# Kernel tuning notes

Measured on AMD Instinct MI355X. Metric: run time of the kernel, lower is better.

## Reference

```python
import jax, jax.numpy as jnp
import numpy as np
from jax import lax

CORR = 16  # corr_size in the original module


def _adaptive_pool16(x):
    # exact adaptive avg pool when H, W divisible by 16 (torch-equivalent)
    B, C, H, W = x.shape
    return x.reshape(B, C, CORR, H // CORR, CORR, W // CORR).mean(axis=(3, 5))


def _l2_normalize(x, eps=1e-12):
    # torch F.normalize default: L2 over dim=1, norm clamped to eps
    n = jnp.sqrt(jnp.sum(x * x, axis=1, keepdims=True))
    return x / jnp.maximum(n, eps)


def _instance_norm(x, eps=1e-5):
    # InstanceNorm2d, affine=False, biased variance over H,W per (b,c)
    mu = x.mean(axis=(2, 3), keepdims=True)
    var = jnp.mean((x - mu) ** 2, axis=(2, 3), keepdims=True)
    return (x - mu) * lax.rsqrt(var + eps)


def _corr_reduce(x, W1, b1, W2, b2):
    # 1x1 conv (256 -> fc) + bias
    y = jnp.einsum('bchw,oc->bohw', x, W1[:, :, 0, 0]) + b1[None, :, None, None]
    y = jax.nn.relu(_instance_norm(y))
    # 3x3 conv, padding=1, stride=1
    y = lax.conv_general_dilated(y, W2, (1, 1), 'SAME',
                                 dimension_numbers=('NCHW', 'OIHW', 'NCHW'))
    return y + b2[None, :, None, None]


def _corr(feat):
    # pooled [B,C,16,16] used as per-sample bank of 256 1x1 conv kernels
    pooled = _adaptive_pool16(feat)                      # [B,C,16,16]
    norm = _l2_normalize(feat)                           # [B,C,H,W]
    B, C = pooled.shape[:2]
    ker = pooled.reshape(B, C, CORR * CORR)              # [B,C,256]
    # corr[b,p,h,w] = sum_c ker[b,c,p] * norm[b,c,h,w]
    return jnp.einsum('bcp,bchw->bphw', ker, norm)


def setup_inputs() -> dict:
    key = jax.random.key(0)
    ks = jax.random.split(key, 6)
    B, C, H, W = 16, 256, 96, 96
    fc = 256
    return {
        'F_infrared': jax.random.normal(ks[0], (B, C, H, W), jnp.float32),
        'F_visible': jax.random.normal(ks[1], (B, C, H, W), jnp.float32),
        'W1': jax.random.normal(ks[2], (fc, CORR * CORR, 1, 1), jnp.float32) * 0.05,
        'b1': jax.random.normal(ks[3], (fc,), jnp.float32) * 0.05,
        'W2': jax.random.normal(ks[4], (fc, fc, 3, 3), jnp.float32) * 0.05,
        'b2': jax.random.normal(ks[5], (fc,), jnp.float32) * 0.05,
    }


def reference(F_infrared, F_visible, W1, b1, W2, b2):
    VIS_corr = _corr_reduce(_corr(F_visible), W1, b1, W2, b2)
    IR_corr = _corr_reduce(_corr(F_infrared), W1, b1, W2, b2)
    return (IR_corr, VIS_corr)
```

## Files before the change

kernel.cpp:

```cpp
#include <hip/hip_runtime.h>
#include <hip/hip_bf16.h>

#define BATCH 16
#define CH    256
#define HH    96
#define WW    96
#define HWSZ  9216
#define FCH   256
#define PP    256

typedef float f32x4 __attribute__((ext_vector_type(4)));
typedef short bf16x8 __attribute__((ext_vector_type(8)));
typedef unsigned short ushortT;

#define APAD_ELEMS 2458624
#define APAD_CHUNKS 307328

__device__ __forceinline__ void gload16(const void* g, void* l) {
    __builtin_amdgcn_global_load_lds((const __attribute__((address_space(1))) void*)g,
                                     (__attribute__((address_space(3))) void*)l, 16, 0, 0);
}
__device__ __forceinline__ float bfu2f(ushortT u) {
    return __uint_as_float(((unsigned)u) << 16);
}
__device__ __forceinline__ ushortT f2bfu(float f) {
    __hip_bfloat16 hb = __float2bfloat16(f);
    return *reinterpret_cast<ushortT*>(&hb);
}

__global__ void fpack_k(const float* __restrict__ feat, ushortT* __restrict__ fpack,
                        float* __restrict__ rnorm)
{
    int b = blockIdx.y;
    int hw = blockIdx.x * 256 + threadIdx.x;
    const float* src = feat + (size_t)b * CH * HWSZ + hw;
    uint4* dst = (uint4*)fpack + (size_t)b * 32 * HWSZ + hw;
    float ss = 0.f;
    for (int cb = 0; cb < 32; ++cb) {
        union { ushortT u[8]; uint4 v; } pk;
#pragma unroll
        for (int i = 0; i < 8; ++i) {
            float v = src[(size_t)(cb * 8 + i) * HWSZ];
            ss += v * v;
            pk.u[i] = f2bfu(v);
        }
        dst[(size_t)cb * HWSZ] = pk.v;
    }
    rnorm[b * HWSZ + hw] = 1.0f / fmaxf(sqrtf(ss), 1e-12f);
}

__global__ void pool16b_k(const ushortT* __restrict__ fpack, float* __restrict__ pooled)
{
    int cb = blockIdx.x, b = blockIdx.y;
    const uint4* fp = (const uint4*)fpack + ((size_t)b * 32 + cb) * HWSZ;
    int t = threadIdx.x;
    int pr = t >> 4, pc = t & 15;
    float s[8] = {};
#pragma unroll
    for (int i = 0; i < 6; ++i) {
#pragma unroll
        for (int j = 0; j < 6; ++j) {
            uint4 v = fp[(pr * 6 + i) * WW + pc * 6 + j];
            const ushortT* u = (const ushortT*)&v;
#pragma unroll
            for (int k = 0; k < 8; ++k) s[k] += bfu2f(u[k]);
        }
    }
#pragma unroll
    for (int k = 0; k < 8; ++k)
        pooled[((size_t)b * CH + cb * 8 + k) * PP + t] = s[k] * (1.0f / 36.0f);
}

__global__ void gemmM_k(const float* __restrict__ W1, const float* __restrict__ pooled,
                        ushortT* __restrict__ Mb16)
{
    int b = blockIdx.z;
    int o0 = blockIdx.y * 16, c0 = blockIdx.x * 16;
    int ty = threadIdx.y, tx = threadIdx.x;
    __shared__ float Ws[16][17], Ps[16][17];
    float acc = 0.f;
    for (int p0 = 0; p0 < PP; p0 += 16) {
        Ws[ty][tx] = W1[(o0 + ty) * PP + p0 + tx];
        Ps[ty][tx] = pooled[((size_t)b * CH + (c0 + ty)) * PP + p0 + tx];
        __syncthreads();
#pragma unroll
        for (int p = 0; p < 16; ++p) acc += Ws[ty][p] * Ps[tx][p];
        __syncthreads();
    }
    int c = c0 + tx, o = o0 + ty;
    Mb16[(((size_t)b * 32 + (c >> 3)) * 256 + o) * 8 + (c & 7)] = f2bfu(acc);
}

__global__ void repack_w2_k(const float* __restrict__ W2, ushortT* __restrict__ W2r2)
{
    int e = blockIdx.x * 256 + threadIdx.x;
    int ci = e & 7, o = (e >> 3) & 255, cb = (e >> 11) & 31, s = e >> 16;
    int c = cb * 8 + ci;
    W2r2[e] = f2bfu(W2[((size_t)o * 256 + c) * 9 + s]);
}

__global__ void zborder_k(uint4* __restrict__ apad)
{
    int bl = blockIdx.x;
    uint4* apC = apad + (size_t)bl * APAD_CHUNKS;
    uint4 z; z.x = 0; z.y = 0; z.z = 0; z.w = 0;
    for (int e = threadIdx.x; e < 3136; e += 256) {
        apC[e] = z;
        apC[(size_t)97 * 32 * 98 + e] = z;
    }
    for (int e = threadIdx.x; e < 3072; e += 256) {
        int row = 1 + (e >> 5), cb = e & 31;
        size_t base = (size_t)(row * 32 + cb) * 98;
        apC[base] = z;
        apC[base + 97] = z;
    }
}

__global__ __launch_bounds__(256, 4) void gemmYm_k(const ushortT* __restrict__ Mb16,
                                                   const ushortT* __restrict__ fpack,
                                                   const float* __restrict__ rnorm,
                                                   ushortT* __restrict__ apad, int b0)
{
    int bl = blockIdx.z, bg = b0 + bl;
    int hw0 = blockIdx.x * 128;
    int o0 = blockIdx.y * 128;
    int tid = threadIdx.x, wave = tid >> 6, lane = tid & 63;
    int wm = wave >> 1, wn = wave & 1;
    int lr = lane & 15, kb = lane >> 4;

    __shared__ __align__(16) char smem[33280];

    const uint4* MbC = (const uint4*)Mb16 + (size_t)bg * 32 * 256;
    const uint4* fpC = (const uint4*)fpack + (size_t)bg * 32 * HWSZ;

    f32x4 acc[4][4] = {};

    auto STAGE = [&](int buf, int s) {
        int cb0 = s * 4;
        uint4* A = (uint4*)smem + (size_t)buf * 1024;
        uint4* B = A + 512;
#pragma unroll
        for (int i = 0; i < 2; ++i) {
            int e = tid + i * 256;
            int kk = e >> 7, j = e & 127;
            gload16(MbC + (size_t)(cb0 + kk) * 256 + o0 + j, A + e);
            gload16(fpC + (size_t)(cb0 + kk) * HWSZ + hw0 + j, B + e);
        }
    };

    STAGE(0, 0);
    for (int s = 0; s < 8; ++s) {
        int buf = s & 1;
        __syncthreads();
        if (s < 7) STAGE(buf ^ 1, s + 1);
        const bf16x8* AsV = (const bf16x8*)(smem + (size_t)buf * 16384);
        const bf16x8* BsV = AsV + 512;
        bf16x8 af[4], bfv[4];
#pragma unroll
        for (int mf = 0; mf < 4; ++mf) af[mf] = AsV[kb * 128 + wm * 64 + mf * 16 + lr];
#pragma unroll
        for (int nf = 0; nf < 4; ++nf) bfv[nf] = BsV[kb * 128 + wn * 64 + nf * 16 + lr];
#pragma unroll
        for (int mf = 0; mf < 4; ++mf)
#pragma unroll
            for (int nf = 0; nf < 4; ++nf)
                acc[mf][nf] = __builtin_amdgcn_mfma_f32_16x16x32_bf16(af[mf], bfv[nf], acc[mf][nf], 0, 0, 0);
    }
    __syncthreads();

    float rn[4];
#pragma unroll
    for (int nf = 0; nf < 4; ++nf)
        rn[nf] = rnorm[(size_t)bg * HWSZ + hw0 + wn * 64 + nf * 16 + lr];

    ushortT* T = (ushortT*)smem;
#pragma unroll
    for (int mf = 0; mf < 4; ++mf)
#pragma unroll
        for (int nf = 0; nf < 4; ++nf)
#pragma unroll
            for (int r = 0; r < 4; ++r)
                T[(wn * 64 + nf * 16 + lr) * 130 + wm * 64 + mf * 16 + kb * 4 + r] =
                    f2bfu(acc[mf][nf][r] * rn[nf]);
    __syncthreads();

    uint4* apC = (uint4*)apad + (size_t)bl * APAD_CHUNKS;
    int ob0 = blockIdx.y * 16;
#pragma unroll
    for (int i = 0; i < 8; ++i) {
        int e = tid + i * 256;
        int hw_l = e >> 4, ob = e & 15;
        uint4 v = *(uint4*)&T[hw_l * 130 + ob * 8];
        int hw = hw0 + hw_l;
        int h = hw / 96, w = hw - h * 96;
        apC[(size_t)((h + 1) * 32 + ob0 + ob) * 98 + (w + 1)] = v;
    }
}

__global__ void instats2_k(const ushortT* __restrict__ apad, float* __restrict__ mu,
                           float* __restrict__ istd)
{
    int ob = blockIdx.x, bl = blockIdx.y;
    const uint4* apC = (const uint4*)apad + (size_t)bl * APAD_CHUNKS;
    float s[8] = {}, s2[8] = {};
    for (int e = threadIdx.x; e < HWSZ; e += 256) {
        int row = e / 96;
        int w = e - row * 96;
        uint4 v = apC[(size_t)((row + 1) * 32 + ob) * 98 + w + 1];
        const ushortT* u = (const ushortT*)&v;
#pragma unroll
        for (int k = 0; k < 8; ++k) {
            float f = bfu2f(u[k]);
            s[k] += f; s2[k] += f * f;
        }
    }
#pragma unroll
    for (int off = 32; off > 0; off >>= 1) {
#pragma unroll
        for (int k = 0; k < 8; ++k) {
            s[k]  += __shfl_down(s[k],  off, 64);
            s2[k] += __shfl_down(s2[k], off, 64);
        }
    }
    __shared__ float sh[4][16];
    int wid = threadIdx.x >> 6;
    if ((threadIdx.x & 63) == 0) {
#pragma unroll
        for (int k = 0; k < 8; ++k) { sh[wid][k] = s[k]; sh[wid][8 + k] = s2[k]; }
    }
    __syncthreads();
    if (threadIdx.x < 8) {
        int k = threadIdx.x;
        float S  = sh[0][k] + sh[1][k] + sh[2][k] + sh[3][k];
        float S2 = sh[0][8 + k] + sh[1][8 + k] + sh[2][8 + k] + sh[3][8 + k];
        float m   = S * (1.0f / HWSZ);
        float var = S2 * (1.0f / HWSZ) - m * m;
        if (var < 0.f) var = 0.f;
        mu[bl * 256 + ob * 8 + k]   = m;
        istd[bl * 256 + ob * 8 + k] = rsqrtf(var + 1e-5f);
    }
}

__global__ void nr_k(ushortT* __restrict__ apad, const float* __restrict__ mu,
                     const float* __restrict__ istd)
{
    int row = blockIdx.x + 1, bl = blockIdx.y;
    __shared__ float smu[256], sis[256];
    smu[threadIdx.x] = mu[bl * 256 + threadIdx.x];
    sis[threadIdx.x] = istd[bl * 256 + threadIdx.x];
    __syncthreads();
    uint4* apC = (uint4*)apad + (size_t)bl * APAD_CHUNKS + (size_t)row * 32 * 98;
    for (int e = threadIdx.x; e < 3072; e += 256) {
        int ob = e / 96;
        int w = e - ob * 96 + 1;
        uint4 v = apC[(size_t)ob * 98 + w];
        ushortT* u = (ushortT*)&v;
#pragma unroll
        for (int k = 0; k < 8; ++k) {
            float f = (bfu2f(u[k]) - smu[ob * 8 + k]) * sis[ob * 8 + k];
            u[k] = f2bfu(f > 0.f ? f : 0.f);
        }
        apC[(size_t)ob * 98 + w] = v;
    }
}

__global__ __launch_bounds__(256, 2) void conv3m4_k(const ushortT* __restrict__ apad,
                                                    const ushortT* __restrict__ W2r2,
                                                    const float* __restrict__ b2,
                                                    float* __restrict__ out)
{
    int h0 = blockIdx.x * 4;
    int o0 = blockIdx.y * 64;
    int bl = blockIdx.z;
    int tid = threadIdx.x;
    int wave = tid >> 6, lane = tid & 63;
    int lr = lane & 15, kb = lane >> 4;

    __shared__ __align__(16) uint4 AsC[2304];
    __shared__ __align__(16) uint4 BsC[2560];

    const uint4* apadC = (const uint4*)apad + (size_t)bl * APAD_CHUNKS;
    const uint4* w2C   = (const uint4*)W2r2;
    const bf16x8* AsV = (const bf16x8*)AsC;
    const bf16x8* BsV = (const bf16x8*)BsC;

    f32x4 acc[4][6] = {};

    for (int ci = 0; ci < 8; ++ci) {
        int cb0 = ci * 4;
        __syncthreads();
#pragma unroll
        for (int i = 0; i < 9; ++i) {
            int e = tid + i * 256;
            int o = e & 63, kk = (e >> 6) & 3, s = e >> 8;
            gload16(w2C + (size_t)(s * 32 + cb0 + kk) * 256 + o0 + o, &AsC[e]);
        }
#pragma unroll
        for (int i = 0; i < 10; ++i) {
            int e = tid + i * 256;
            int se = e < 2352 ? e : e - 256;
            int w = se % 98, r = se / 98;
            int kk = r & 3, row = r >> 2;
            gload16(apadC + (size_t)((h0 + row) * 32 + cb0 + kk) * 98 + w, &BsC[e]);
        }
        __syncthreads();
#pragma unroll
        for (int kh = 0; kh < 3; ++kh) {
#pragma unroll
            for (int kw = 0; kw < 3; ++kw) {
                int s = kh * 3 + kw;
                bf16x8 af[4];
#pragma unroll
                for (int mf = 0; mf < 4; ++mf)
                    af[mf] = AsV[(s * 4 + kb) * 64 + mf * 16 + lr];
#pragma unroll
                for (int nf = 0; nf < 6; ++nf) {
                    bf16x8 bfr = BsV[((wave + kh) * 4 + kb) * 98 + nf * 16 + lr + kw];
#pragma unroll
                    for (int mf = 0; mf < 4; ++mf)
                        acc[mf][nf] = __builtin_amdgcn_mfma_f32_16x16x32_bf16(af[mf], bfr, acc[mf][nf], 0, 0, 0);
                }
            }
        }
    }

    int h = h0 + wave;
    float* obase = out + (size_t)bl * FCH * HWSZ + (size_t)h * WW;
#pragma unroll
    for (int mf = 0; mf < 4; ++mf) {
#pragma unroll
        for (int r = 0; r < 4; ++r) {
            int o = o0 + mf * 16 + kb * 4 + r;
            float bias = b2[o];
            float* orow = obase + (size_t)o * HWSZ;
#pragma unroll
            for (int nf = 0; nf < 6; ++nf)
                orow[nf * 16 + lr] = acc[mf][nf][r] + bias;
        }
    }
}

extern "C" void kernel_launch(void* const* d_in, const int* in_sizes, int n_in,
                              void* d_out, int out_size, void* d_ws, size_t ws_size,
                              hipStream_t stream)
{
    const float* Fir  = (const float*)d_in[0];
    const float* Fvis = (const float*)d_in[1];
    const float* W1   = (const float*)d_in[2];
    const float* W2   = (const float*)d_in[4];
    const float* b2   = (const float*)d_in[5];
    float* out = (float*)d_out;

    char* w = (char*)d_ws;
    const size_t poolB = (size_t)BATCH * CH * PP * 4;
    const size_t MbB   = (size_t)BATCH * 32 * 256 * 8 * 2;
    const size_t rnB   = (size_t)BATCH * HWSZ * 4;
    const size_t stB   = (size_t)BATCH * FCH * 4;
    const size_t w2rB  = (size_t)9 * 32 * 256 * 8 * 2;
    const size_t fpB   = (size_t)BATCH * 32 * HWSZ * 8 * 2;

    size_t off = 0;
    float*   pooled = (float*)(w + off);   off += poolB;
    ushortT* Mb16   = (ushortT*)(w + off); off += MbB;
    float*   rnorm  = (float*)(w + off);   off += rnB;
    float*   mu     = (float*)(w + off);   off += stB;
    float*   istd   = (float*)(w + off);   off += stB;
    ushortT* W2r2   = (ushortT*)(w + off); off += w2rB;
    ushortT* fpack  = (ushortT*)(w + off); off += fpB;
    const size_t fixed = off;

    const size_t apadB = (size_t)APAD_ELEMS * 2;
    size_t avail = ws_size > fixed ? ws_size - fixed : 0;
    int NB = (int)(avail / apadB);
    if (NB > BATCH) NB = BATCH;
    if (NB < 1) NB = 1;
    ushortT* apad = (ushortT*)(w + fixed);

    repack_w2_k<<<2304, 256, 0, stream>>>(W2, W2r2);
    zborder_k<<<NB, 256, 0, stream>>>((uint4*)apad);

    for (int f = 0; f < 2; ++f) {
        const float* feat = (f == 0) ? Fir : Fvis;
        float* o_ = out + (size_t)f * BATCH * FCH * HWSZ;

        fpack_k<<<dim3(36, BATCH), 256, 0, stream>>>(feat, fpack, rnorm);
        pool16b_k<<<dim3(32, BATCH), 256, 0, stream>>>(fpack, pooled);
        gemmM_k<<<dim3(16, 16, BATCH), dim3(16, 16), 0, stream>>>(W1, pooled, Mb16);

        for (int b0 = 0; b0 < BATCH; b0 += NB) {
            int nb = BATCH - b0 < NB ? BATCH - b0 : NB;
            gemmYm_k<<<dim3(72, 2, nb), 256, 0, stream>>>(Mb16, fpack, rnorm, apad, b0);
            instats2_k<<<dim3(32, nb), 256, 0, stream>>>(apad, mu, istd);
            nr_k<<<dim3(96, nb), 256, 0, stream>>>(apad, mu, istd);
            conv3m4_k<<<dim3(24, 4, nb), 256, 0, stream>>>(apad, W2r2, b2,
                                                           o_ + (size_t)b0 * FCH * HWSZ);
        }
    }
}
```

Before: 637.4 us.

## Fuse instance-norm stats into GEMM epilogue, load conv weights to registers, swizzle blocks

The GEMM epilogue now writes per-tile partial sums and sums of squares, which a small finalize kernel reduces. This replaces the separate stats kernel that re-read the whole padded activation buffer. The 3x3 conv kernel stops staging weights in LDS and loads them straight from global memory into registers per kh, which reduces LDS use but adds global loads inside the inner loop. It also remaps block indices so each XCD works on two batches, for L2 locality. Stats are now computed from fp32 values before bf16 rounding, which changes numerics slightly.

```diff
diff --git a/kernel.cpp b/kernel.cpp
--- a/kernel.cpp
+++ b/kernel.cpp
@@ -119,7 +119,9 @@
 __global__ __launch_bounds__(256, 4) void gemmYm_k(const ushortT* __restrict__ Mb16,
                                                    const ushortT* __restrict__ fpack,
                                                    const float* __restrict__ rnorm,
-                                                   ushortT* __restrict__ apad, int b0)
+                                                   ushortT* __restrict__ apad,
+                                                   float* __restrict__ ps,
+                                                   float* __restrict__ ps2, int b0)
 {
     int bl = blockIdx.z, bg = b0 + bl;
     int hw0 = blockIdx.x * 128;
@@ -173,6 +175,39 @@
     for (int nf = 0; nf < 4; ++nf)
         rn[nf] = rnorm[(size_t)bg * HWSZ + hw0 + wn * 64 + nf * 16 + lr];
 
+    {
+        float sA[4][4], sB[4][4];
+#pragma unroll
+        for (int mf = 0; mf < 4; ++mf)
+#pragma unroll
+            for (int r = 0; r < 4; ++r) {
+                float s1 = 0.f, s2 = 0.f;
+#pragma unroll
+                for (int nf = 0; nf < 4; ++nf) {
+                    float v = acc[mf][nf][r] * rn[nf];
+                    s1 += v; s2 += v * v;
+                }
+#pragma unroll
+                for (int off = 8; off > 0; off >>= 1) {
+                    s1 += __shfl_down(s1, off, 16);
+                    s2 += __shfl_down(s2, off, 16);
+                }
+                sA[mf][r] = s1; sB[mf][r] = s2;
+            }
+        if (lr == 0) {
+            int col = blockIdx.x * 2 + wn;
+#pragma unroll
+            for (int mf = 0; mf < 4; ++mf)
+#pragma unroll
+                for (int r = 0; r < 4; ++r) {
+                    int og = o0 + wm * 64 + mf * 16 + kb * 4 + r;
+                    size_t idx = ((size_t)bl * 256 + og) * 144 + col;
+                    ps[idx]  = sA[mf][r];
+                    ps2[idx] = sB[mf][r];
+                }
+        }
+    }
+
     ushortT* T = (ushortT*)smem;
 #pragma unroll
     for (int mf = 0; mf < 4; ++mf)
@@ -197,48 +232,19 @@
     }
 }
 
-__global__ void instats2_k(const ushortT* __restrict__ apad, float* __restrict__ mu,
-                           float* __restrict__ istd)
-{
-    int ob = blockIdx.x, bl = blockIdx.y;
-    const uint4* apC = (const uint4*)apad + (size_t)bl * APAD_CHUNKS;
-    float s[8] = {}, s2[8] = {};
-    for (int e = threadIdx.x; e < HWSZ; e += 256) {
-        int row = e / 96;
-        int w = e - row * 96;
-        uint4 v = apC[(size_t)((row + 1) * 32 + ob) * 98 + w + 1];
-        const ushortT* u = (const ushortT*)&v;
-#pragma unroll
-        for (int k = 0; k < 8; ++k) {
-            float f = bfu2f(u[k]);
-            s[k] += f; s2[k] += f * f;
-        }
-    }
-#pragma unroll
-    for (int off = 32; off > 0; off >>= 1) {
-#pragma unroll
-        for (int k = 0; k < 8; ++k) {
-            s[k]  += __shfl_down(s[k],  off, 64);
-            s2[k] += __shfl_down(s2[k], off, 64);
-        }
-    }
-    __shared__ float sh[4][16];
-    int wid = threadIdx.x >> 6;
-    if ((threadIdx.x & 63) == 0) {
-#pragma unroll
-        for (int k = 0; k < 8; ++k) { sh[wid][k] = s[k]; sh[wid][8 + k] = s2[k]; }
-    }
-    __syncthreads();
-    if (threadIdx.x < 8) {
-        int k = threadIdx.x;
-        float S  = sh[0][k] + sh[1][k] + sh[2][k] + sh[3][k];
-        float S2 = sh[0][8 + k] + sh[1][8 + k] + sh[2][8 + k] + sh[3][8 + k];
-        float m   = S * (1.0f / HWSZ);
-        float var = S2 * (1.0f / HWSZ) - m * m;
-        if (var < 0.f) var = 0.f;
-        mu[bl * 256 + ob * 8 + k]   = m;
-        istd[bl * 256 + ob * 8 + k] = rsqrtf(var + 1e-5f);
-    }
+__global__ void finstats_k(const float* __restrict__ ps, const float* __restrict__ ps2,
+                           float* __restrict__ mu, float* __restrict__ istd)
+{
+    int bl = blockIdx.x, o = threadIdx.x;
+    const float* p1 = ps  + ((size_t)bl * 256 + o) * 144;
+    const float* p2 = ps2 + ((size_t)bl * 256 + o) * 144;
+    float S = 0.f, S2 = 0.f;
+    for (int i = 0; i < 144; ++i) { S += p1[i]; S2 += p2[i]; }
+    float m   = S * (1.0f / HWSZ);
+    float var = S2 * (1.0f / HWSZ) - m * m;
+    if (var < 0.f) var = 0.f;
+    mu[bl * 256 + o]   = m;
+    istd[bl * 256 + o] = rsqrtf(var + 1e-5f);
 }
 
 __global__ void nr_k(ushortT* __restrict__ apad, const float* __restrict__ mu,
@@ -264,61 +270,66 @@
     }
 }
 
-__global__ __launch_bounds__(256, 2) void conv3m4_k(const ushortT* __restrict__ apad,
+__global__ __launch_bounds__(256, 2) void conv3m7_k(const ushortT* __restrict__ apad,
                                                     const ushortT* __restrict__ W2r2,
                                                     const float* __restrict__ b2,
-                                                    float* __restrict__ out)
-{
-    int h0 = blockIdx.x * 4;
-    int o0 = blockIdx.y * 64;
-    int bl = blockIdx.z;
+                                                    float* __restrict__ out, int swz)
+{
+    int ht, ot, bl;
+    if (swz) {
+        int lin = blockIdx.x + 24 * (blockIdx.y + 4 * blockIdx.z);
+        int xcd = lin & 7, i = lin >> 3;
+        int second = (i >= 96) ? 1 : 0;
+        bl = 2 * xcd + second;
+        int w = i - second * 96;
+        ot = w / 24; ht = w - ot * 24;
+    } else {
+        ht = blockIdx.x; ot = blockIdx.y; bl = blockIdx.z;
+    }
+    int h0 = ht * 4;
+    int o0 = ot * 64;
     int tid = threadIdx.x;
     int wave = tid >> 6, lane = tid & 63;
     int lr = lane & 15, kb = lane >> 4;
 
-    __shared__ __align__(16) uint4 AsC[2304];
     __shared__ __align__(16) uint4 BsC[2560];
 
     const uint4* apadC = (const uint4*)apad + (size_t)bl * APAD_CHUNKS;
-    const uint4* w2C   = (const uint4*)W2r2;
-    const bf16x8* AsV = (const bf16x8*)AsC;
-    const bf16x8* BsV = (const bf16x8*)BsC;
+    const bf16x8* w2V  = (const bf16x8*)W2r2;
+    const bf16x8* BsV  = (const bf16x8*)BsC;
 
     f32x4 acc[4][6] = {};
 
     for (int ci = 0; ci < 8; ++ci) {
         int cb0 = ci * 4;
         __syncthreads();
-#pragma unroll
-        for (int i = 0; i < 9; ++i) {
-            int e = tid + i * 256;
-            int o = e & 63, kk = (e >> 6) & 3, s = e >> 8;
-            gload16(w2C + (size_t)(s * 32 + cb0 + kk) * 256 + o0 + o, &AsC[e]);
-        }
 #pragma unroll
         for (int i = 0; i < 10; ++i) {
             int e = tid + i * 256;
             int se = e < 2352 ? e : e - 256;
             int w = se % 98, r = se / 98;
             int kk = r & 3, row = r >> 2;
-            gload16(apadC + (size_t)((h0 + row) * 32 + cb0 + kk) * 98 + w, &BsC[e]);
+            gload16(apadC + (size_t)((h0 + row) * 32 + cb0 + kk) * 98 + w,
+                    &BsC[e]);
         }
         __syncthreads();
-#pragma unroll
+#pragma unroll 1
         for (int kh = 0; kh < 3; ++kh) {
+            bf16x8 aR[3][4];
+#pragma unroll
+            for (int kw = 0; kw < 3; ++kw)
+#pragma unroll
+                for (int mf = 0; mf < 4; ++mf)
+                    aR[kw][mf] = w2V[(size_t)((kh * 3 + kw) * 32 + cb0 + kb) * 256
+                                     + o0 + mf * 16 + lr];
 #pragma unroll
             for (int kw = 0; kw < 3; ++kw) {
-                int s = kh * 3 + kw;
-                bf16x8 af[4];
-#pragma unroll
-                for (int mf = 0; mf < 4; ++mf)
-                    af[mf] = AsV[(s * 4 + kb) * 64 + mf * 16 + lr];
 #pragma unroll
                 for (int nf = 0; nf < 6; ++nf) {
                     bf16x8 bfr = BsV[((wave + kh) * 4 + kb) * 98 + nf * 16 + lr + kw];
 #pragma unroll
                     for (int mf = 0; mf < 4; ++mf)
-                        acc[mf][nf] = __builtin_amdgcn_mfma_f32_16x16x32_bf16(af[mf], bfr, acc[mf][nf], 0, 0, 0);
+                        acc[mf][nf] = __builtin_amdgcn_mfma_f32_16x16x32_bf16(aR[kw][mf], bfr, acc[mf][nf], 0, 0, 0);
                 }
             }
         }
@@ -357,6 +368,7 @@
     const size_t rnB   = (size_t)BATCH * HWSZ * 4;
     const size_t stB   = (size_t)BATCH * FCH * 4;
     const size_t w2rB  = (size_t)9 * 32 * 256 * 8 * 2;
+    const size_t psB   = (size_t)BATCH * 256 * 144 * 4;
     const size_t fpB   = (size_t)BATCH * 32 * HWSZ * 8 * 2;
 
     size_t off = 0;
@@ -366,6 +378,8 @@
     float*   mu     = (float*)(w + off);   off += stB;
     float*   istd   = (float*)(w + off);   off += stB;
     ushortT* W2r2   = (ushortT*)(w + off); off += w2rB;
+    float*   ps     = (float*)(w + off);   off += psB;
+    float*   ps2    = (float*)(w + off);   off += psB;
     ushortT* fpack  = (ushortT*)(w + off); off += fpB;
     const size_t fixed = off;
 
@@ -389,11 +403,13 @@
 
         for (int b0 = 0; b0 < BATCH; b0 += NB) {
             int nb = BATCH - b0 < NB ? BATCH - b0 : NB;
-            gemmYm_k<<<dim3(72, 2, nb), 256, 0, stream>>>(Mb16, fpack, rnorm, apad, b0);
-            instats2_k<<<dim3(32, nb), 256, 0, stream>>>(apad, mu, istd);
+            gemmYm_k<<<dim3(72, 2, nb), 256, 0, stream>>>(Mb16, fpack, rnorm, apad,
+                                                          ps, ps2, b0);
+            finstats_k<<<nb, 256, 0, stream>>>(ps, ps2, mu, istd);
             nr_k<<<dim3(96, nb), 256, 0, stream>>>(apad, mu, istd);
-            conv3m4_k<<<dim3(24, 4, nb), 256, 0, stream>>>(apad, W2r2, b2,
-                                                           o_ + (size_t)b0 * FCH * HWSZ);
-        }
-    }
-}
+            conv3m7_k<<<dim3(24, 4, nb), 256, 0, stream>>>(apad, W2r2, b2,
+                                                           o_ + (size_t)b0 * FCH * HWSZ,
+                                                           nb == 16 ? 1 : 0);
+        }
+    }
+}
```

New measurement: 719.8 us. 1.13x slower.
